# Kernel optimization log

Measured on AMD Instinct MI355X. Metric: run time of the kernel, lower is better.

The kernel has to match this reference:

```python
import jax, jax.numpy as jnp
import numpy as np

B, T, H = 128, 512, 1024          # batch, seq_len, rnn_hidden_dim
S, K, HID = 128, 64, 512          # state_dim, num_states, hidden_dims[0]
D = H + S                         # inference GRU input dim


def setup_inputs() -> dict:
    key = jax.random.key(0)
    ks = jax.random.split(key, 8)
    contexts = jax.random.normal(ks[0], (B, T, H), jnp.float32)
    init = jax.random.uniform(ks[1], (B, K), jnp.float32)
    initial_state = init / init.sum(-1, keepdims=True)  # valid distribution
    # state embeddings ~ N(0, 0.1)
    E = 0.1 * jax.random.normal(ks[2], (K, S), jnp.float32)
    # PyTorch GRU default init: U(-1/sqrt(H), 1/sqrt(H))
    sc = 1.0 / np.sqrt(H)
    W_ih = jax.random.uniform(ks[3], (3 * H, D), jnp.float32, -sc, sc)
    W_hh = jax.random.uniform(ks[4], (3 * H, H), jnp.float32, -sc, sc)
    b_ih = jnp.zeros((3 * H,), jnp.float32)
    b_hh = jnp.zeros((3 * H,), jnp.float32)
    # output projection: xavier_normal weights, zero biases
    W1 = jax.random.normal(ks[5], (HID, H), jnp.float32) * np.sqrt(2.0 / (H + HID))
    b1 = jnp.zeros((HID,), jnp.float32)
    W2 = jax.random.normal(ks[6], (K, HID), jnp.float32) * np.sqrt(2.0 / (HID + K))
    b2 = jnp.zeros((K,), jnp.float32)
    return dict(contexts=contexts, initial_state=initial_state, E=E,
                W_ih=W_ih, W_hh=W_hh, b_ih=b_ih, b_hh=b_hh,
                W1=W1, b1=b1, W2=W2, b2=b2)


def reference(contexts, initial_state, E, W_ih, W_hh, b_ih, b_hh, W1, b1, W2, b2):
    """forward_sequence: per-timestep GRU recurrence with soft state embedding."""
    def step(carry, x_t):  # x_t: [B, H]
        h, prev_state = carry
        emb = prev_state @ E                       # [B, S] soft state embedding
        x = jnp.concatenate([x_t, emb], axis=-1)   # [B, H+S]
        gi = x @ W_ih.T + b_ih                     # [B, 3H]
        gh = h @ W_hh.T + b_hh                     # [B, 3H]
        i_r, i_z, i_n = jnp.split(gi, 3, axis=-1)
        h_r, h_z, h_n = jnp.split(gh, 3, axis=-1)
        r = jax.nn.sigmoid(i_r + h_r)
        z = jax.nn.sigmoid(i_z + h_z)
        n = jnp.tanh(i_n + r * h_n)
        h_new = (1.0 - z) * n + z * h              # PyTorch GRUCell update
        logits = jnp.tanh(h_new @ W1.T + b1) @ W2.T + b2  # [B, K]
        new_state = jax.nn.softmax(jnp.clip(logits, -10.0, 10.0), axis=-1)
        return (h_new, new_state), logits

    h0 = jnp.zeros((contexts.shape[0], W_hh.shape[1]), contexts.dtype)
    xs = jnp.swapaxes(contexts, 0, 1)              # [T, B, H]
    _, logits = jax.lax.scan(step, (h0, initial_state), xs)
    return jnp.swapaxes(logits, 0, 1)              # [B, T, K]
```

## Files before the change

### kernel.cpp

```cpp
#include <hip/hip_runtime.h>
#include <stdint.h>

#define Bb 128
#define Tt 512
#define Hh 1024
#define Ss 128
#define Kk 64
#define HID 512
#define G3 3072
#define Dd 1152
#define KC 256
#define LSTRA 264
#define LSTRS 72

typedef short bf16x8 __attribute__((ext_vector_type(8)));
typedef float f32x4 __attribute__((ext_vector_type(4)));
typedef unsigned int u32x4v __attribute__((ext_vector_type(4)));
#define MFMA16 __builtin_amdgcn_mfma_f32_16x16x32_bf16

#define CTR(i) (ctrl + (i) * 32)

__device__ __forceinline__ unsigned short f2bf(float f) {
  union { float f; unsigned u; } v; v.f = f;
  unsigned u = v.u;
  u += 0x7fffu + ((u >> 16) & 1u);
  return (unsigned short)(u >> 16);
}
__device__ __forceinline__ float sigm(float x) { return 1.f / (1.f + __expf(-x)); }
__device__ __forceinline__ float tanh_f(float x) {
  x = fminf(15.f, fmaxf(-15.f, x));
  float e = __expf(2.f * x);
  return (e - 1.f) / (e + 1.f);
}

__device__ __forceinline__ void cload8(u32x4v o[8], const void* p, int sb) {
  const char* c = (const char*)p;
  asm volatile(
    "global_load_dwordx4 %0, %8, off sc0 sc1\n\t"
    "global_load_dwordx4 %1, %9, off sc0 sc1\n\t"
    "global_load_dwordx4 %2, %10, off sc0 sc1\n\t"
    "global_load_dwordx4 %3, %11, off sc0 sc1\n\t"
    "global_load_dwordx4 %4, %12, off sc0 sc1\n\t"
    "global_load_dwordx4 %5, %13, off sc0 sc1\n\t"
    "global_load_dwordx4 %6, %14, off sc0 sc1\n\t"
    "global_load_dwordx4 %7, %15, off sc0 sc1\n\t"
    "s_waitcnt vmcnt(0)"
    : "=&v"(o[0]), "=&v"(o[1]), "=&v"(o[2]), "=&v"(o[3]),
      "=&v"(o[4]), "=&v"(o[5]), "=&v"(o[6]), "=&v"(o[7])
    : "v"(c), "v"(c + sb), "v"(c + 2 * sb), "v"(c + 3 * sb),
      "v"(c + 4 * sb), "v"(c + 5 * sb), "v"(c + 6 * sb), "v"(c + 7 * sb)
    : "memory");
}
__device__ __forceinline__ void cload2(u32x4v o[2], const void* p, int sb) {
  const char* c = (const char*)p;
  asm volatile(
    "global_load_dwordx4 %0, %2, off sc0 sc1\n\t"
    "global_load_dwordx4 %1, %3, off sc0 sc1\n\t"
    "s_waitcnt vmcnt(0)"
    : "=&v"(o[0]), "=&v"(o[1])
    : "v"(c), "v"(c + sb)
    : "memory");
}
__device__ __forceinline__ void cloadf4(float o[4], const float* p, int sb) {
  const char* c = (const char*)p;
  asm volatile(
    "global_load_dword %0, %4, off sc0 sc1\n\t"
    "global_load_dword %1, %5, off sc0 sc1\n\t"
    "global_load_dword %2, %6, off sc0 sc1\n\t"
    "global_load_dword %3, %7, off sc0 sc1\n\t"
    "s_waitcnt vmcnt(0)"
    : "=&v"(o[0]), "=&v"(o[1]), "=&v"(o[2]), "=&v"(o[3])
    : "v"(c), "v"(c + sb), "v"(c + 2 * sb), "v"(c + 3 * sb)
    : "memory");
}

__device__ __forceinline__ void rel_add(int* p) {
  __syncthreads();
  if (threadIdx.x == 0)
    __hip_atomic_fetch_add(p, 1, __ATOMIC_RELEASE, __HIP_MEMORY_SCOPE_AGENT);
}
__device__ __forceinline__ void wait_ge(int* p, int target) {
  __syncthreads();
  if (threadIdx.x == 0) {
    while (__hip_atomic_load(p, __ATOMIC_RELAXED, __HIP_MEMORY_SCOPE_AGENT) < target)
      __builtin_amdgcn_s_sleep(1);
  }
  __syncthreads();
}

__global__ void __launch_bounds__(256) prep_convert(const float* Whh, const float* Wih,
    const float* W1, const float* W2,
    unsigned short* WhhB, unsigned short* WXB, unsigned short* W1B, unsigned short* W2B) {
  const int n0 = G3 * Hh;
  const int n1 = n0 + G3 * Hh;
  const int n2 = n1 + HID * Hh;
  const int n3 = n2 + Kk * HID;
  for (int i = blockIdx.x * 256 + threadIdx.x; i < n3; i += gridDim.x * 256) {
    if (i < n0) WhhB[i] = f2bf(Whh[i]);
    else if (i < n1) { int j = i - n0; int n = j >> 10, k = j & 1023; WXB[j] = f2bf(Wih[n * Dd + k]); }
    else if (i < n2) { int j = i - n1; W1B[j] = f2bf(W1[j]); }
    else { int j = i - n2; W2B[j] = f2bf(W2[j]); }
  }
}
__global__ void __launch_bounds__(256) prep_mt(const float* Wih, const float* E, unsigned short* MtB) {
  int gid = blockIdx.x * 256 + threadIdx.x;
  if (gid >= G3 * Kk) return;
  int n = gid >> 6, kk = gid & 63;
  const float* wp = Wih + (size_t)n * Dd + Hh;
  const float* ep = E + kk * Ss;
  float s = 0.f;
  for (int t = 0; t < Ss; ++t) s += wp[t] * ep[t];
  MtB[n * Kk + kk] = f2bf(s);
}

__device__ void a_main(int bid, const float* init_state, const float* b_ih, const float* b_hh,
    const unsigned short* WhhB, const unsigned short* MtB,
    float* h32, unsigned short* hbf, const float* gix, const unsigned short* sbuf,
    int* ctrl, unsigned short* sA, unsigned short* sB, unsigned short* sS) {
  const int tid = threadIdx.x;
  const int wv = tid >> 6, ln = tid & 63;
  const int mh = bid >> 6, jg = bid & 63;
  const int m0 = mh * 64, j0 = jg * 16;
  const int al = ln & 15, q = ln >> 4, koff = q * 8;
  const int j = j0 + al;
  const float bir = b_ih[j], biz = b_ih[Hh + j], bin_ = b_ih[2 * Hh + j];
  const float bhr = b_hh[j], bhz = b_hh[Hh + j], bhn = b_hh[2 * Hh + j];

  for (int t = 0; t < Tt; ++t) {
    f32x4 accR = {0,0,0,0}, accZ = {0,0,0,0}, accNH = {0,0,0,0}, accNS = {0,0,0,0};

    if (t > 0) {
      wait_ge(CTR(5), 128 * t);
      const unsigned short* hb = hbf + ((t - 1) & 1) * (Bb * Hh);
      const int ra = tid >> 5, c8 = (tid & 31) * 8;
      for (int kc = 0; kc < 4; ++kc) {
        const int k0 = kc * KC;
        __syncthreads();
        {
          u32x4v tmp[8];
          cload8(tmp, hb + (m0 + ra) * Hh + k0 + c8, 8 * Hh * 2);
#pragma unroll
          for (int u = 0; u < 8; ++u)
            *(u32x4v*)&sA[(ra + 8 * u) * LSTRA + c8] = tmp[u];
        }
        {
          int ch = tid;
#pragma unroll
          for (int u = 0; u < 6; ++u, ch += 256) {
            int r = ch >> 5, cc = (ch & 31) * 8;
            int g = r >> 4, rr = r & 15;
            *(u32x4v*)&sB[r * LSTRA + cc] = *(const u32x4v*)(WhhB + (g * Hh + j0 + rr) * Hh + k0 + cc);
          }
        }
        __syncthreads();
#pragma unroll
        for (int ks = 0; ks < 8; ++ks) {
          bf16x8 af  = *(bf16x8*)&sA[(wv * 16 + al) * LSTRA + ks * 32 + koff];
          bf16x8 b0  = *(bf16x8*)&sB[(al) * LSTRA + ks * 32 + koff];
          bf16x8 b1v = *(bf16x8*)&sB[(16 + al) * LSTRA + ks * 32 + koff];
          bf16x8 b2v = *(bf16x8*)&sB[(32 + al) * LSTRA + ks * 32 + koff];
          accR  = MFMA16(af, b0,  accR, 0, 0, 0);
          accZ  = MFMA16(af, b1v, accZ, 0, 0, 0);
          accNH = MFMA16(af, b2v, accNH, 0, 0, 0);
        }
      }
    }

    wait_ge(CTR(1), 64 * (t + 1));
    float gxr[4], gxz[4], gxn[4];
    {
      const float* gp = gix + (t & 1) * (Bb * G3) + (size_t)(m0 + wv * 16 + q * 4) * G3;
      cloadf4(gxr, gp + j, G3 * 4);
      cloadf4(gxz, gp + Hh + j, G3 * 4);
      cloadf4(gxn, gp + 2 * Hh + j, G3 * 4);
    }

    __syncthreads();
    if (t > 0) {
      wait_ge(CTR(4), 8 * t);
      const unsigned short* sb = sbuf + ((t - 1) & 1) * (Bb * Kk);
      u32x4v tmp[2];
      cload2(tmp, sb + (m0 + (tid >> 3)) * Kk + (tid & 7) * 8, 32 * Kk * 2);
      *(u32x4v*)&sS[(tid >> 3) * LSTRS + (tid & 7) * 8] = tmp[0];
      *(u32x4v*)&sS[((tid >> 3) + 32) * LSTRS + (tid & 7) * 8] = tmp[1];
    } else {
      for (int e = tid; e < 4096; e += 256) {
        int r = e >> 6, k = e & 63;
        sS[r * LSTRS + k] = f2bf(init_state[(m0 + r) * Kk + k]);
      }
    }
    for (int ch = tid; ch < 384; ch += 256) {
      int r = ch >> 3, cc = (ch & 7) * 8;
      int g = r >> 4, rr = r & 15;
      *(u32x4v*)&sB[r * LSTRA + cc] = *(const u32x4v*)(MtB + (g * Hh + j0 + rr) * Kk + cc);
    }
    __syncthreads();
#pragma unroll
    for (int ks = 0; ks < 2; ++ks) {
      bf16x8 af  = *(bf16x8*)&sS[(wv * 16 + al) * LSTRS + ks * 32 + koff];
      bf16x8 b0  = *(bf16x8*)&sB[(al) * LSTRA + ks * 32 + koff];
      bf16x8 b1v = *(bf16x8*)&sB[(16 + al) * LSTRA + ks * 32 + koff];
      bf16x8 b2v = *(bf16x8*)&sB[(32 + al) * LSTRA + ks * 32 + koff];
      accR  = MFMA16(af, b0,  accR, 0, 0, 0);
      accZ  = MFMA16(af, b1v, accZ, 0, 0, 0);
      accNS = MFMA16(af, b2v, accNS, 0, 0, 0);
    }

    const float* hp = h32 + ((t + 1) & 1) * (Bb * Hh);
    float* hc = h32 + (t & 1) * (Bb * Hh);
    unsigned short* hbc = hbf + (t & 1) * (Bb * Hh);
#pragma unroll
    for (int i = 0; i < 4; ++i) {
      const int m = m0 + wv * 16 + q * 4 + i;
      float gr  = accR[i] + gxr[i] + bir + bhr;
      float gz  = accZ[i] + gxz[i] + biz + bhz;
      float hn  = accNH[i] + bhn;
      float in_ = accNS[i] + gxn[i] + bin_;
      float r = sigm(gr), z = sigm(gz);
      float n = tanh_f(in_ + r * hn);
      float hprev = (t > 0) ? hp[m * Hh + j] : 0.f;
      float hnew = (1.f - z) * n + z * hprev;
      hc[m * Hh + j] = hnew;
      hbc[m * Hh + j] = f2bf(hnew);
    }
    rel_add(CTR(5));
  }
}

__device__ void x_main(int xg, const float* ctx, unsigned short* xbf,
    const unsigned short* WXB, float* gix, int* ctrl,
    unsigned short* sA, unsigned short* sB) {
  const int tid = threadIdx.x;
  const int wv = tid >> 6, ln = tid & 63;
  const int al = ln & 15, q = ln >> 4, koff = q * 8;
  const int c0 = xg * 48;

  for (int tt = 0; tt < Tt; ++tt) {
    if (tt >= 2) wait_ge(CTR(1), 64 * (tt - 1));
    unsigned short* xb = xbf + (tt & 1) * (Bb * Hh);
    {
      int i4beg = xg * 512 + tid;
#pragma unroll
      for (int u = 0; u < 2; ++u) {
        int e = (i4beg + u * 256) * 4;
        int m = e >> 10, hh = e & 1023;
        const float4 v = *(const float4*)(ctx + (size_t)m * (Tt * Hh) + (size_t)tt * Hh + hh);
        ushort4 o;
        o.x = f2bf(v.x); o.y = f2bf(v.y); o.z = f2bf(v.z); o.w = f2bf(v.w);
        *(ushort4*)(xb + e) = o;
      }
    }
    rel_add(CTR(2));
    wait_ge(CTR(2), 64 * (tt + 1));

    f32x4 a00 = {0,0,0,0}, a01 = {0,0,0,0}, a02 = {0,0,0,0};
    f32x4 a10 = {0,0,0,0}, a11 = {0,0,0,0}, a12 = {0,0,0,0};
    const int ra = tid >> 5, c8 = (tid & 31) * 8;
    for (int kc = 0; kc < 4; ++kc) {
      const int k0 = kc * KC;
      __syncthreads();
      {
        u32x4v tmp[8];
        cload8(tmp, xb + ra * Hh + k0 + c8, 8 * Hh * 2);
#pragma unroll
        for (int u = 0; u < 8; ++u)
          *(u32x4v*)&sA[(ra + 8 * u) * LSTRA + c8] = tmp[u];
        u32x4v tmp2[8];
        cload8(tmp2, xb + (64 + ra) * Hh + k0 + c8, 8 * Hh * 2);
#pragma unroll
        for (int u = 0; u < 8; ++u)
          *(u32x4v*)&sA[(64 + ra + 8 * u) * LSTRA + c8] = tmp2[u];
      }
      {
        int ch = tid;
#pragma unroll
        for (int u = 0; u < 6; ++u, ch += 256) {
          int r = ch >> 5, cc = (ch & 31) * 8;
          *(u32x4v*)&sB[r * LSTRA + cc] = *(const u32x4v*)(WXB + (c0 + r) * Hh + k0 + cc);
        }
      }
      __syncthreads();
#pragma unroll
      for (int ks = 0; ks < 8; ++ks) {
        bf16x8 a0  = *(bf16x8*)&sA[(wv * 32 + al) * LSTRA + ks * 32 + koff];
        bf16x8 a1  = *(bf16x8*)&sA[(wv * 32 + 16 + al) * LSTRA + ks * 32 + koff];
        bf16x8 b0  = *(bf16x8*)&sB[al * LSTRA + ks * 32 + koff];
        bf16x8 b1v = *(bf16x8*)&sB[(16 + al) * LSTRA + ks * 32 + koff];
        bf16x8 b2v = *(bf16x8*)&sB[(32 + al) * LSTRA + ks * 32 + koff];
        a00 = MFMA16(a0, b0,  a00, 0, 0, 0);
        a01 = MFMA16(a0, b1v, a01, 0, 0, 0);
        a02 = MFMA16(a0, b2v, a02, 0, 0, 0);
        a10 = MFMA16(a1, b0,  a10, 0, 0, 0);
        a11 = MFMA16(a1, b1v, a11, 0, 0, 0);
        a12 = MFMA16(a1, b2v, a12, 0, 0, 0);
      }
    }
    if (tt >= 2) wait_ge(CTR(5), 128 * (tt - 1));
    float* go = gix + (tt & 1) * (Bb * G3);
#pragma unroll
    for (int i = 0; i < 4; ++i) {
      int mb = wv * 32 + q * 4 + i;
      go[mb * G3 + c0 + al] = a00[i];
      go[mb * G3 + c0 + 16 + al] = a01[i];
      go[mb * G3 + c0 + 32 + al] = a02[i];
      go[(mb + 16) * G3 + c0 + al] = a10[i];
      go[(mb + 16) * G3 + c0 + 16 + al] = a11[i];
      go[(mb + 16) * G3 + c0 + 32 + al] = a12[i];
    }
    rel_add(CTR(1));
  }
}

__device__ void al_main(int ag, const unsigned short* hbf,
    const unsigned short* W1B, const unsigned short* W2B, const float* b1, const float* b2,
    unsigned short* abf, unsigned short* sbuf, float* dout, int* ctrl,
    unsigned short* sA, unsigned short* sB, unsigned short* sS) {
  const int tid = threadIdx.x;
  const int wv = tid >> 6, ln = tid & 63;
  const int al = ln & 15, q = ln >> 4, koff = q * 8;
  const int c0 = (ag >> 1) * 16;
  const int rh = (ag & 1) * 64;
  const float b1v = b1[c0 + al];
  const float b2v = b2[wv * 16 + al];
  float* sE = (float*)sS;
  float* sInv = (float*)(sS + 4416);

  for (int s = 0; s < Tt; ++s) {
    wait_ge(CTR(5), 128 * (s + 1));
    if (s >= 2) wait_ge(CTR(4), 8 * (s - 1));
    const unsigned short* hb = hbf + (s & 1) * (Bb * Hh);
    unsigned short* ab = abf + (s & 1) * (Bb * HID);

    f32x4 aa = {0,0,0,0};
    const int ra = tid >> 5, c8 = (tid & 31) * 8;
    for (int kc = 0; kc < 4; ++kc) {
      const int k0 = kc * KC;
      __syncthreads();
      {
        u32x4v tmp[8];
        cload8(tmp, hb + (rh + ra) * Hh + k0 + c8, 8 * Hh * 2);
#pragma unroll
        for (int u = 0; u < 8; ++u)
          *(u32x4v*)&sA[(ra + 8 * u) * LSTRA + c8] = tmp[u];
      }
      {
        int ch = tid;
#pragma unroll
        for (int u = 0; u < 2; ++u, ch += 256) {
          int r = ch >> 5, cc = (ch & 31) * 8;
          *(u32x4v*)&sB[r * LSTRA + cc] = *(const u32x4v*)(W1B + (c0 + r) * Hh + k0 + cc);
        }
      }
      __syncthreads();
#pragma unroll
      for (int ks = 0; ks < 8; ++ks) {
        bf16x8 a0 = *(bf16x8*)&sA[(wv * 16 + al) * LSTRA + ks * 32 + koff];
        bf16x8 b0 = *(bf16x8*)&sB[al * LSTRA + ks * 32 + koff];
        aa = MFMA16(a0, b0, aa, 0, 0, 0);
      }
    }
#pragma unroll
    for (int i = 0; i < 4; ++i) {
      int mb = rh + wv * 16 + q * 4 + i;
      ab[mb * HID + c0 + al] = f2bf(tanh_f(aa[i] + b1v));
    }
    rel_add(CTR(3));

    if (ag < 8) {
      wait_ge(CTR(3), 64 * (s + 1));
      const int r0 = ag * 16;
      f32x4 lg = {0,0,0,0};
      for (int kc = 0; kc < 2; ++kc) {
        const int k0 = kc * KC;
        __syncthreads();
        {
          u32x4v tmp[2];
          cload2(tmp, ab + (r0 + ra) * HID + k0 + c8, 8 * HID * 2);
          *(u32x4v*)&sA[ra * LSTRA + c8] = tmp[0];
          *(u32x4v*)&sA[(ra + 8) * LSTRA + c8] = tmp[1];
        }
        {
          int ch = tid;
#pragma unroll
          for (int u = 0; u < 8; ++u, ch += 256) {
            int r = ch >> 5, cc = (ch & 31) * 8;
            *(u32x4v*)&sB[r * LSTRA + cc] = *(const u32x4v*)(W2B + r * HID + k0 + cc);
          }
        }
        __syncthreads();
#pragma unroll
        for (int ks = 0; ks < 8; ++ks) {
          bf16x8 af  = *(bf16x8*)&sA[al * LSTRA + ks * 32 + koff];
          bf16x8 bf_ = *(bf16x8*)&sB[(wv * 16 + al) * LSTRA + ks * 32 + koff];
          lg = MFMA16(af, bf_, lg, 0, 0, 0);
        }
      }
      float vraw[4], ev[4];
#pragma unroll
      for (int i = 0; i < 4; ++i) {
        float v = lg[i] + b2v;
        vraw[i] = v;
        float c = fminf(10.f, fmaxf(-10.f, v));
        ev[i] = __expf(c);
        sE[(q * 4 + i) * 68 + (wv * 16 + al)] = ev[i];
      }
      __syncthreads();
      if (tid < 16) {
        const float* row = &sE[tid * 68];
        float sm = 0.f;
        for (int k = 0; k < 64; ++k) sm += row[k];
        sInv[tid] = 1.f / sm;
      }
      __syncthreads();
      const int col = wv * 16 + al;
      unsigned short* sb = sbuf + (s & 1) * (Bb * Kk);
#pragma unroll
      for (int i = 0; i < 4; ++i) {
        int row16 = q * 4 + i;
        int grow = r0 + row16;
        dout[grow * (Tt * Kk) + s * Kk + col] = vraw[i];
        sb[grow * Kk + col] = f2bf(ev[i] * sInv[row16]);
      }
      rel_add(CTR(4));
    }
  }
}

__global__ void __launch_bounds__(256, 1)
seqkern(const float* ctx, const float* init_state, const float* b_ih, const float* b_hh,
        const float* b1, const float* b2, float* dout,
        const unsigned short* WhhB, const unsigned short* WXB, const unsigned short* W1B,
        const unsigned short* W2B, const unsigned short* MtB,
        float* h32, unsigned short* hbf, float* gix, unsigned short* xbf,
        unsigned short* abf, unsigned short* sbuf, int* ctrl) {
  extern __shared__ char smem[];
  unsigned short* sA = (unsigned short*)smem;
  unsigned short* sB = (unsigned short*)(smem + 67584);
  unsigned short* sS = (unsigned short*)(smem + 101376);
  const int bid = blockIdx.x;
  if (bid < 128)
    a_main(bid, init_state, b_ih, b_hh, WhhB, MtB, h32, hbf, gix, sbuf, ctrl, sA, sB, sS);
  else if (bid < 192)
    x_main(bid - 128, ctx, xbf, WXB, gix, ctrl, sA, sB);
  else
    al_main(bid - 192, hbf, W1B, W2B, b1, b2, abf, sbuf, dout, ctrl, sA, sB, sS);
}

extern "C" void kernel_launch(void* const* d_in, const int* in_sizes, int n_in,
                              void* d_out, int out_size, void* d_ws, size_t ws_size,
                              hipStream_t stream) {
  const float* ctx        = (const float*)d_in[0];
  const float* init_state = (const float*)d_in[1];
  const float* E          = (const float*)d_in[2];
  const float* Wih        = (const float*)d_in[3];
  const float* Whh        = (const float*)d_in[4];
  const float* b_ih       = (const float*)d_in[5];
  const float* b_hh       = (const float*)d_in[6];
  const float* W1         = (const float*)d_in[7];
  const float* b1         = (const float*)d_in[8];
  const float* W2         = (const float*)d_in[9];
  const float* b2         = (const float*)d_in[10];
  float* out = (float*)d_out;
  (void)in_sizes; (void)n_in; (void)out_size; (void)ws_size;

  char* ws = (char*)d_ws;
  size_t off = 0;
  auto take = [&](size_t sz) { char* p = ws + off; off += (sz + 255) & ~(size_t)255; return p; };
  int* ctrl             = (int*)take(1024);
  unsigned short* WhhB  = (unsigned short*)take((size_t)G3 * Hh * 2);
  unsigned short* WXB   = (unsigned short*)take((size_t)G3 * Hh * 2);
  unsigned short* W1B   = (unsigned short*)take((size_t)HID * Hh * 2);
  unsigned short* W2B   = (unsigned short*)take((size_t)Kk * HID * 2);
  unsigned short* MtB   = (unsigned short*)take((size_t)G3 * Kk * 2);
  float* h32            = (float*)take((size_t)2 * Bb * Hh * 4);
  unsigned short* hbf   = (unsigned short*)take((size_t)2 * Bb * Hh * 2);
  float* gix            = (float*)take((size_t)2 * Bb * G3 * 4);
  unsigned short* xbf   = (unsigned short*)take((size_t)2 * Bb * Hh * 2);
  unsigned short* abf   = (unsigned short*)take((size_t)2 * Bb * HID * 2);
  unsigned short* sbuf  = (unsigned short*)take((size_t)2 * Bb * Kk * 2);

  hipMemsetAsync(ctrl, 0, 1024, stream);
  hipLaunchKernelGGL(prep_convert, dim3(2048), dim3(256), 0, stream,
                     Whh, Wih, W1, W2, WhhB, WXB, W1B, W2B);
  hipLaunchKernelGGL(prep_mt, dim3(768), dim3(256), 0, stream, Wih, E, MtB);

  static int smem_set = 0;
  if (!smem_set) {
    hipFuncSetAttribute((const void*)seqkern,
                        hipFuncAttributeMaxDynamicSharedMemorySize, 110592);
    smem_set = 1;
  }
  void* args[] = {(void*)&ctx, (void*)&init_state, (void*)&b_ih, (void*)&b_hh,
                  (void*)&b1, (void*)&b2, (void*)&out,
                  (void*)&WhhB, (void*)&WXB, (void*)&W1B, (void*)&W2B, (void*)&MtB,
                  (void*)&h32, (void*)&hbf, (void*)&gix, (void*)&xbf,
                  (void*)&abf, (void*)&sbuf, (void*)&ctrl};
  hipLaunchCooperativeKernel((const void*)seqkern, dim3(256), dim3(256), args, 110592, stream);
}
```

Measured before the change: 16.86 ms.

## Keep recurrent and projection weight slices resident in LDS across timesteps

Each persistent block of the recurrent GRU, as well as the output-projection blocks, now loads its W_hh, Mt, W1 and W2 weight slices into shared memory once before the time loop, rather than reloading them from global memory every timestep. Dynamic shared memory grows to about 148 KB to fit the resident weights, which MI355X LDS can hold. The twelve gate-input loads are also merged into one batched asm load with a single wait. Less global and L2 traffic sits on the sequential critical path, in exchange for higher LDS use per block.

```diff
diff --git a/kernel.cpp b/kernel.cpp
--- a/kernel.cpp
+++ b/kernel.cpp
@@ -61,16 +61,29 @@
     : "v"(c), "v"(c + sb)
     : "memory");
 }
-__device__ __forceinline__ void cloadf4(float o[4], const float* p, int sb) {
-  const char* c = (const char*)p;
+__device__ __forceinline__ void cloadf12(float o[12],
+    const float* a0, const float* a1, const float* a2, const float* a3,
+    const float* a4, const float* a5, const float* a6, const float* a7,
+    const float* a8, const float* a9, const float* a10, const float* a11) {
   asm volatile(
-    "global_load_dword %0, %4, off sc0 sc1\n\t"
-    "global_load_dword %1, %5, off sc0 sc1\n\t"
-    "global_load_dword %2, %6, off sc0 sc1\n\t"
-    "global_load_dword %3, %7, off sc0 sc1\n\t"
+    "global_load_dword %0, %12, off sc0 sc1\n\t"
+    "global_load_dword %1, %13, off sc0 sc1\n\t"
+    "global_load_dword %2, %14, off sc0 sc1\n\t"
+    "global_load_dword %3, %15, off sc0 sc1\n\t"
+    "global_load_dword %4, %16, off sc0 sc1\n\t"
+    "global_load_dword %5, %17, off sc0 sc1\n\t"
+    "global_load_dword %6, %18, off sc0 sc1\n\t"
+    "global_load_dword %7, %19, off sc0 sc1\n\t"
+    "global_load_dword %8, %20, off sc0 sc1\n\t"
+    "global_load_dword %9, %21, off sc0 sc1\n\t"
+    "global_load_dword %10, %22, off sc0 sc1\n\t"
+    "global_load_dword %11, %23, off sc0 sc1\n\t"
     "s_waitcnt vmcnt(0)"
-    : "=&v"(o[0]), "=&v"(o[1]), "=&v"(o[2]), "=&v"(o[3])
-    : "v"(c), "v"(c + sb), "v"(c + 2 * sb), "v"(c + 3 * sb)
+    : "=&v"(o[0]), "=&v"(o[1]), "=&v"(o[2]), "=&v"(o[3]),
+      "=&v"(o[4]), "=&v"(o[5]), "=&v"(o[6]), "=&v"(o[7]),
+      "=&v"(o[8]), "=&v"(o[9]), "=&v"(o[10]), "=&v"(o[11])
+    : "v"(a0), "v"(a1), "v"(a2), "v"(a3), "v"(a4), "v"(a5),
+      "v"(a6), "v"(a7), "v"(a8), "v"(a9), "v"(a10), "v"(a11)
     : "memory");
 }
 
@@ -116,7 +129,11 @@
 __device__ void a_main(int bid, const float* init_state, const float* b_ih, const float* b_hh,
     const unsigned short* WhhB, const unsigned short* MtB,
     float* h32, unsigned short* hbf, const float* gix, const unsigned short* sbuf,
-    int* ctrl, unsigned short* sA, unsigned short* sB, unsigned short* sS) {
+    int* ctrl, char* smem) {
+  unsigned short* sA  = (unsigned short*)smem;
+  unsigned short* sBp = (unsigned short*)(smem + 33792);
+  unsigned short* sMt = (unsigned short*)(smem + 135168);
+  unsigned short* sS  = (unsigned short*)(smem + 142080);
   const int tid = threadIdx.x;
   const int wv = tid >> 6, ln = tid & 63;
   const int mh = bid >> 6, jg = bid & 63;
@@ -126,6 +143,24 @@
   const float bir = b_ih[j], biz = b_ih[Hh + j], bin_ = b_ih[2 * Hh + j];
   const float bhr = b_hh[j], bhz = b_hh[Hh + j], bhn = b_hh[2 * Hh + j];
 
+  for (int kc = 0; kc < 4; ++kc) {
+    const int k0 = kc * KC;
+    unsigned short* sB = sBp + kc * (48 * LSTRA);
+    int ch = tid;
+#pragma unroll
+    for (int u = 0; u < 6; ++u, ch += 256) {
+      int r = ch >> 5, cc = (ch & 31) * 8;
+      int g = r >> 4, rr = r & 15;
+      *(u32x4v*)&sB[r * LSTRA + cc] = *(const u32x4v*)(WhhB + (g * Hh + j0 + rr) * Hh + k0 + cc);
+    }
+  }
+  for (int ch = tid; ch < 384; ch += 256) {
+    int r = ch >> 3, cc = (ch & 7) * 8;
+    int g = r >> 4, rr = r & 15;
+    *(u32x4v*)&sMt[r * LSTRS + cc] = *(const u32x4v*)(MtB + (g * Hh + j0 + rr) * Kk + cc);
+  }
+  __syncthreads();
+
   for (int t = 0; t < Tt; ++t) {
     f32x4 accR = {0,0,0,0}, accZ = {0,0,0,0}, accNH = {0,0,0,0}, accNS = {0,0,0,0};
 
@@ -135,6 +170,7 @@
       const int ra = tid >> 5, c8 = (tid & 31) * 8;
       for (int kc = 0; kc < 4; ++kc) {
         const int k0 = kc * KC;
+        const unsigned short* sB = sBp + kc * (48 * LSTRA);
         __syncthreads();
         {
           u32x4v tmp[8];
@@ -142,15 +178,6 @@
 #pragma unroll
           for (int u = 0; u < 8; ++u)
             *(u32x4v*)&sA[(ra + 8 * u) * LSTRA + c8] = tmp[u];
-        }
-        {
-          int ch = tid;
-#pragma unroll
-          for (int u = 0; u < 6; ++u, ch += 256) {
-            int r = ch >> 5, cc = (ch & 31) * 8;
-            int g = r >> 4, rr = r & 15;
-            *(u32x4v*)&sB[r * LSTRA + cc] = *(const u32x4v*)(WhhB + (g * Hh + j0 + rr) * Hh + k0 + cc);
-          }
         }
         __syncthreads();
 #pragma unroll
@@ -167,12 +194,14 @@
     }
 
     wait_ge(CTR(1), 64 * (t + 1));
-    float gxr[4], gxz[4], gxn[4];
+    float gx[12];
     {
-      const float* gp = gix + (t & 1) * (Bb * G3) + (size_t)(m0 + wv * 16 + q * 4) * G3;
-      cloadf4(gxr, gp + j, G3 * 4);
-      cloadf4(gxz, gp + Hh + j, G3 * 4);
-      cloadf4(gxn, gp + 2 * Hh + j, G3 * 4);
+      const float* gp = gix + (t & 1) * (Bb * G3) + (size_t)(m0 + wv * 16 + q * 4) * G3 + j;
+      cloadf12(gx,
+        gp,          gp + Hh,          gp + 2 * Hh,
+        gp + G3,     gp + G3 + Hh,     gp + G3 + 2 * Hh,
+        gp + 2 * G3, gp + 2 * G3 + Hh, gp + 2 * G3 + 2 * Hh,
+        gp + 3 * G3, gp + 3 * G3 + Hh, gp + 3 * G3 + 2 * Hh);
     }
 
     __syncthreads();
@@ -189,18 +218,13 @@
         sS[r * LSTRS + k] = f2bf(init_state[(m0 + r) * Kk + k]);
       }
     }
-    for (int ch = tid; ch < 384; ch += 256) {
-      int r = ch >> 3, cc = (ch & 7) * 8;
-      int g = r >> 4, rr = r & 15;
-      *(u32x4v*)&sB[r * LSTRA + cc] = *(const u32x4v*)(MtB + (g * Hh + j0 + rr) * Kk + cc);
-    }
     __syncthreads();
 #pragma unroll
     for (int ks = 0; ks < 2; ++ks) {
       bf16x8 af  = *(bf16x8*)&sS[(wv * 16 + al) * LSTRS + ks * 32 + koff];
-      bf16x8 b0  = *(bf16x8*)&sB[(al) * LSTRA + ks * 32 + koff];
-      bf16x8 b1v = *(bf16x8*)&sB[(16 + al) * LSTRA + ks * 32 + koff];
-      bf16x8 b2v = *(bf16x8*)&sB[(32 + al) * LSTRA + ks * 32 + koff];
+      bf16x8 b0  = *(bf16x8*)&sMt[(al) * LSTRS + ks * 32 + koff];
+      bf16x8 b1v = *(bf16x8*)&sMt[(16 + al) * LSTRS + ks * 32 + koff];
+      bf16x8 b2v = *(bf16x8*)&sMt[(32 + al) * LSTRS + ks * 32 + koff];
       accR  = MFMA16(af, b0,  accR, 0, 0, 0);
       accZ  = MFMA16(af, b1v, accZ, 0, 0, 0);
       accNS = MFMA16(af, b2v, accNS, 0, 0, 0);
@@ -212,10 +236,10 @@
 #pragma unroll
     for (int i = 0; i < 4; ++i) {
       const int m = m0 + wv * 16 + q * 4 + i;
-      float gr  = accR[i] + gxr[i] + bir + bhr;
-      float gz  = accZ[i] + gxz[i] + biz + bhz;
+      float gr  = accR[i] + gx[i * 3 + 0] + bir + bhr;
+      float gz  = accZ[i] + gx[i * 3 + 1] + biz + bhz;
       float hn  = accNH[i] + bhn;
-      float in_ = accNS[i] + gxn[i] + bin_;
+      float in_ = accNS[i] + gx[i * 3 + 2] + bin_;
       float r = sigm(gr), z = sigm(gz);
       float n = tanh_f(in_ + r * hn);
       float hprev = (t > 0) ? hp[m * Hh + j] : 0.f;
@@ -313,8 +337,12 @@
 
 __device__ void al_main(int ag, const unsigned short* hbf,
     const unsigned short* W1B, const unsigned short* W2B, const float* b1, const float* b2,
-    unsigned short* abf, unsigned short* sbuf, float* dout, int* ctrl,
-    unsigned short* sA, unsigned short* sB, unsigned short* sS) {
+    unsigned short* abf, unsigned short* sbuf, float* dout, int* ctrl, char* smem) {
+  unsigned short* sA  = (unsigned short*)smem;
+  unsigned short* sW1 = (unsigned short*)(smem + 33792);
+  unsigned short* sW2 = (unsigned short*)(smem + 67584);
+  float* sE   = (float*)(smem + 135168);
+  float* sInv = sE + 16 * 68;
   const int tid = threadIdx.x;
   const int wv = tid >> 6, ln = tid & 63;
   const int al = ln & 15, q = ln >> 4, koff = q * 8;
@@ -322,8 +350,30 @@
   const int rh = (ag & 1) * 64;
   const float b1v = b1[c0 + al];
   const float b2v = b2[wv * 16 + al];
-  float* sE = (float*)sS;
-  float* sInv = (float*)(sS + 4416);
+
+  for (int kc = 0; kc < 4; ++kc) {
+    const int k0 = kc * KC;
+    unsigned short* sB = sW1 + kc * (16 * LSTRA);
+    int ch = tid;
+#pragma unroll
+    for (int u = 0; u < 2; ++u, ch += 256) {
+      int r = ch >> 5, cc = (ch & 31) * 8;
+      *(u32x4v*)&sB[r * LSTRA + cc] = *(const u32x4v*)(W1B + (c0 + r) * Hh + k0 + cc);
+    }
+  }
+  if (ag < 8) {
+    for (int kc = 0; kc < 2; ++kc) {
+      const int k0 = kc * KC;
+      unsigned short* sB = sW2 + kc * (64 * LSTRA);
+      int ch = tid;
+#pragma unroll
+      for (int u = 0; u < 8; ++u, ch += 256) {
+        int r = ch >> 5, cc = (ch & 31) * 8;
+        *(u32x4v*)&sB[r * LSTRA + cc] = *(const u32x4v*)(W2B + r * HID + k0 + cc);
+      }
+    }
+  }
+  __syncthreads();
 
   for (int s = 0; s < Tt; ++s) {
     wait_ge(CTR(5), 128 * (s + 1));
@@ -335,6 +385,7 @@
     const int ra = tid >> 5, c8 = (tid & 31) * 8;
     for (int kc = 0; kc < 4; ++kc) {
       const int k0 = kc * KC;
+      const unsigned short* sB = sW1 + kc * (16 * LSTRA);
       __syncthreads();
       {
         u32x4v tmp[8];
@@ -342,14 +393,6 @@
 #pragma unroll
         for (int u = 0; u < 8; ++u)
           *(u32x4v*)&sA[(ra + 8 * u) * LSTRA + c8] = tmp[u];
-      }
-      {
-        int ch = tid;
-#pragma unroll
-        for (int u = 0; u < 2; ++u, ch += 256) {
-          int r = ch >> 5, cc = (ch & 31) * 8;
-          *(u32x4v*)&sB[r * LSTRA + cc] = *(const u32x4v*)(W1B + (c0 + r) * Hh + k0 + cc);
-        }
       }
       __syncthreads();
 #pragma unroll
@@ -372,20 +415,13 @@
       f32x4 lg = {0,0,0,0};
       for (int kc = 0; kc < 2; ++kc) {
         const int k0 = kc * KC;
+        const unsigned short* sB = sW2 + kc * (64 * LSTRA);
         __syncthreads();
         {
           u32x4v tmp[2];
           cload2(tmp, ab + (r0 + ra) * HID + k0 + c8, 8 * HID * 2);
           *(u32x4v*)&sA[ra * LSTRA + c8] = tmp[0];
           *(u32x4v*)&sA[(ra + 8) * LSTRA + c8] = tmp[1];
-        }
-        {
-          int ch = tid;
-#pragma unroll
-          for (int u = 0; u < 8; ++u, ch += 256) {
-            int r = ch >> 5, cc = (ch & 31) * 8;
-            *(u32x4v*)&sB[r * LSTRA + cc] = *(const u32x4v*)(W2B + r * HID + k0 + cc);
-          }
         }
         __syncthreads();
 #pragma unroll
@@ -434,16 +470,14 @@
         float* h32, unsigned short* hbf, float* gix, unsigned short* xbf,
         unsigned short* abf, unsigned short* sbuf, int* ctrl) {
   extern __shared__ char smem[];
-  unsigned short* sA = (unsigned short*)smem;
-  unsigned short* sB = (unsigned short*)(smem + 67584);
-  unsigned short* sS = (unsigned short*)(smem + 101376);
   const int bid = blockIdx.x;
   if (bid < 128)
-    a_main(bid, init_state, b_ih, b_hh, WhhB, MtB, h32, hbf, gix, sbuf, ctrl, sA, sB, sS);
+    a_main(bid, init_state, b_ih, b_hh, WhhB, MtB, h32, hbf, gix, sbuf, ctrl, smem);
   else if (bid < 192)
-    x_main(bid - 128, ctx, xbf, WXB, gix, ctrl, sA, sB);
+    x_main(bid - 128, ctx, xbf, WXB, gix, ctrl,
+           (unsigned short*)smem, (unsigned short*)(smem + 67584));
   else
-    al_main(bid - 192, hbf, W1B, W2B, b1, b2, abf, sbuf, dout, ctrl, sA, sB, sS);
+    al_main(bid - 192, hbf, W1B, W2B, b1, b2, abf, sbuf, dout, ctrl, smem);
 }
 
 extern "C" void kernel_launch(void* const* d_in, const int* in_sizes, int n_in,
@@ -487,7 +521,7 @@
   static int smem_set = 0;
   if (!smem_set) {
     hipFuncSetAttribute((const void*)seqkern,
-                        hipFuncAttributeMaxDynamicSharedMemorySize, 110592);
+                        hipFuncAttributeMaxDynamicSharedMemorySize, 151296);
     smem_set = 1;
   }
   void* args[] = {(void*)&ctx, (void*)&init_state, (void*)&b_ih, (void*)&b_hh,
@@ -495,5 +529,5 @@
                   (void*)&WhhB, (void*)&WXB, (void*)&W1B, (void*)&W2B, (void*)&MtB,
                   (void*)&h32, (void*)&hbf, (void*)&gix, (void*)&xbf,
                   (void*)&abf, (void*)&sbuf, (void*)&ctrl};
-  hipLaunchCooperativeKernel((const void*)seqkern, dim3(256), dim3(256), args, 110592, stream);
-}
+  hipLaunchCooperativeKernel((const void*)seqkern, dim3(256), dim3(256), args, 151296, stream);
+}
```

Measured after the change: 15.45 ms. -8.4%, faster.
